# Performance work log

Measured on AMD Instinct MI355X. Metric: run time of the kernel, lower is better.

## Reference

```python
import jax, jax.numpy as jnp
import numpy as np

NUM_HEADS = 16
ROPE_BASE = 10000.0


def _rope_cos_sin(seq_len, head_dim, dtype):
    # half-split RoPE tables, shape [1, S, 1, head_dim]
    inv_freq = 1.0 / (ROPE_BASE ** (jnp.arange(0, head_dim, 2, dtype=jnp.float32) / head_dim))
    ang = jnp.arange(seq_len, dtype=jnp.float32)[:, None] * inv_freq[None, :]  # [S, hd/2]
    cos = jnp.concatenate([jnp.cos(ang), jnp.cos(ang)], axis=-1)[None, :, None, :]
    sin = jnp.concatenate([jnp.sin(ang), jnp.sin(ang)], axis=-1)[None, :, None, :]
    return cos.astype(dtype), sin.astype(dtype)


def _rotate_half(t):
    h = t.shape[-1] // 2
    return jnp.concatenate([-t[..., h:], t[..., :h]], axis=-1)


def setup_inputs() -> dict:
    key = jax.random.key(0)
    ks = jax.random.split(key, 5)
    B, S, D = 2, 2048, 1024
    std = 1.0 / np.sqrt(D)
    return {
        "x": jax.random.normal(ks[0], (B, S, D), dtype=jnp.float32),
        "Wqkv": jax.random.normal(ks[1], (D, 3 * D), dtype=jnp.float32) * std,
        "bqkv": jax.random.normal(ks[2], (3 * D,), dtype=jnp.float32) * 0.02,
        "Wproj": jax.random.normal(ks[3], (D, D), dtype=jnp.float32) * std,
        "bproj": jax.random.normal(ks[4], (D,), dtype=jnp.float32) * 0.02,
    }


def reference(x, Wqkv, bqkv, Wproj, bproj):
    B, S, D = x.shape
    H = NUM_HEADS
    hd = D // H
    scale = hd ** (-0.5)

    # fused QKV projection, then split: [B, S, 3, H, hd]
    qkv = (jnp.einsum("bsd,de->bse", x, Wqkv) + bqkv).reshape(B, S, 3, H, hd)
    q, k, v = qkv[:, :, 0], qkv[:, :, 1], qkv[:, :, 2]  # each [B, S, H, hd]

    # rotary embedding on q, k
    cos, sin = _rope_cos_sin(S, hd, x.dtype)
    q = q * cos + _rotate_half(q) * sin
    k = k * cos + _rotate_half(k) * sin

    # scaled dot-product attention (non-causal, matching flash-attn default here)
    scores = jnp.einsum("bqhd,bkhd->bhqk", q, k) * scale  # [B, H, S, S]
    probs = jax.nn.softmax(scores, axis=-1)
    o = jnp.einsum("bhqk,bkhd->bqhd", probs, v).reshape(B, S, D)

    # output projection
    return jnp.einsum("bsd,de->bse", o, Wproj) + bproj
```

## Files before the change

### kernel.cpp

```cpp
#include <hip/hip_runtime.h>

typedef unsigned short u16;
typedef unsigned int   u32;
typedef __bf16 bf16x8 __attribute__((ext_vector_type(8)));
typedef float  f32x4  __attribute__((ext_vector_type(4)));
typedef float  f32x16 __attribute__((ext_vector_type(16)));
typedef u32    u32x4  __attribute__((ext_vector_type(4)));

__device__ __forceinline__ u16 f2bf(float f) {
  u32 u = __builtin_bit_cast(u32, f);
  u += 0x7fffu + ((u >> 16) & 1u);
  return (u16)(u >> 16);
}

#define GLOAD_LDS16(gptr, lptr)                                              \
  __builtin_amdgcn_global_load_lds(                                          \
      (const __attribute__((address_space(1))) void*)(gptr),                 \
      (__attribute__((address_space(3))) void*)(lptr), 16, 0, 0)

__global__ __launch_bounds__(256) void cast_x_kernel(const float* __restrict__ x,
                                                     u16* __restrict__ xb, int n4) {
  int i = blockIdx.x * 256 + threadIdx.x;
  if (i >= n4) return;
  const float4 v = ((const float4*)x)[i];
  uint2 o;
  o.x = (u32)f2bf(v.x) | ((u32)f2bf(v.y) << 16);
  o.y = (u32)f2bf(v.z) | ((u32)f2bf(v.w) << 16);
  ((uint2*)xb)[i] = o;
}

__global__ __launch_bounds__(256) void transpose_cast_kernel(const float* __restrict__ W,
                                                             u16* __restrict__ Wt,
                                                             int K, int N) {
  __shared__ float tile[32][33];
  const int k0 = blockIdx.y * 32, n0 = blockIdx.x * 32;
  const int tx = threadIdx.x & 31, ty = threadIdx.x >> 5;
#pragma unroll
  for (int i = 0; i < 32; i += 8)
    tile[ty + i][tx] = W[(size_t)(k0 + ty + i) * N + n0 + tx];
  __syncthreads();
#pragma unroll
  for (int i = 0; i < 32; i += 8)
    Wt[(size_t)(n0 + ty + i) * K + k0 + tx] = f2bf(tile[tx][ty + i]);
}

__global__ __launch_bounds__(256) void gemm_bias_kernel(const u16* __restrict__ A,
                                                        const u16* __restrict__ Bt,
                                                        const float* __restrict__ bias,
                                                        float* __restrict__ C,
                                                        int M, int N, int K) {
  __shared__ u16 As[128][64];
  __shared__ u16 Bs[128][64];
  const int bm = blockIdx.y, bn = blockIdx.x;
  const int tid = threadIdx.x;
  const int wave = tid >> 6, lane = tid & 63;
  const int wr = wave >> 1, wc = wave & 1;
  const int l15 = lane & 15, lhi = lane >> 4;
  f32x4 acc[4][4] = {};

  const size_t arow0 = (size_t)bm * 128, brow0 = (size_t)bn * 128;
  const int srow_in = lane >> 3;
  const int sslot   = (lane & 7) ^ srow_in;

  for (int k0 = 0; k0 < K; k0 += 64) {
#pragma unroll
    for (int i = 0; i < 4; i++) {
      const int r = wave * 32 + i * 8 + srow_in;
      GLOAD_LDS16(A  + (arow0 + r) * K + k0 + sslot * 8, &As[wave * 32 + i * 8][0]);
      GLOAD_LDS16(Bt + (brow0 + r) * K + k0 + sslot * 8, &Bs[wave * 32 + i * 8][0]);
    }
    __syncthreads();

    bf16x8 af[4][2], bfr[4][2];
#pragma unroll
    for (int m = 0; m < 4; m++) {
      const int r = wr * 64 + m * 16 + l15;
#pragma unroll
      for (int kk = 0; kk < 2; kk++)
        af[m][kk] = *(const bf16x8*)(&As[0][0] + r * 64 + (((kk * 4 + lhi) ^ (r & 7)) * 8));
    }
#pragma unroll
    for (int n = 0; n < 4; n++) {
      const int r = wc * 64 + n * 16 + l15;
#pragma unroll
      for (int kk = 0; kk < 2; kk++)
        bfr[n][kk] = *(const bf16x8*)(&Bs[0][0] + r * 64 + (((kk * 4 + lhi) ^ (r & 7)) * 8));
    }
#pragma unroll
    for (int m = 0; m < 4; m++)
#pragma unroll
      for (int n = 0; n < 4; n++) {
        acc[m][n] = __builtin_amdgcn_mfma_f32_16x16x32_bf16(af[m][0], bfr[n][0], acc[m][n], 0, 0, 0);
        acc[m][n] = __builtin_amdgcn_mfma_f32_16x16x32_bf16(af[m][1], bfr[n][1], acc[m][n], 0, 0, 0);
      }
    __syncthreads();
  }
#pragma unroll
  for (int n = 0; n < 4; n++) {
    int col = bn * 128 + wc * 64 + n * 16 + l15;
    float bv = bias[col];
#pragma unroll
    for (int m = 0; m < 4; m++)
#pragma unroll
      for (int r = 0; r < 4; r++) {
        int row = bm * 128 + wr * 64 + m * 16 + lhi * 4 + r;
        C[(size_t)row * N + col] = acc[m][n][r] + bv;
      }
  }
}

#define QK_FOLD 0.18033688011112042f
__global__ __launch_bounds__(256) void rope_qk_kernel(const float* __restrict__ qkv,
                                                      u16* __restrict__ qb,
                                                      u16* __restrict__ kb) {
  const int bs = blockIdx.x;
  const int s = bs & 2047, b = bs >> 11;
  const float* base = qkv + (size_t)bs * 3072;
#pragma unroll
  for (int p = threadIdx.x; p < 512; p += 256) {
    const int h = p >> 5, i = p & 31;
    float inv = exp2f(-13.287712379549449f * (float)i * (1.0f / 32.0f));
    float ang = (float)s * inv;
    float sn, cs;
    sincosf(ang, &sn, &cs);
    float q0 = base[h * 64 + i], q1 = base[h * 64 + i + 32];
    float k0 = base[1024 + h * 64 + i], k1 = base[1024 + h * 64 + i + 32];
    size_t o = ((size_t)(b * 16 + h) * 2048 + s) * 64;
    qb[o + i]      = f2bf((q0 * cs - q1 * sn) * QK_FOLD);
    qb[o + i + 32] = f2bf((q1 * cs + q0 * sn) * QK_FOLD);
    kb[o + i]      = f2bf(k0 * cs - k1 * sn);
    kb[o + i + 32] = f2bf(k1 * cs + k0 * sn);
  }
}

__global__ __launch_bounds__(256) void v_trans_kernel(const float* __restrict__ qkv,
                                                      u16* __restrict__ vt) {
  __shared__ u16 tile[64][65];
  const int blk = blockIdx.x;
  const int st = blk & 31, h = (blk >> 5) & 15, b = blk >> 9;
  const int s0 = st * 64;
  const int t = threadIdx.x;
  const int r = t >> 2, c0 = (t & 3) * 16;
  const float* src = qkv + (size_t)(b * 2048 + s0 + r) * 3072 + 2048 + h * 64 + c0;
#pragma unroll
  for (int j = 0; j < 16; j++) tile[r][c0 + j] = f2bf(src[j]);
  __syncthreads();
  u16* dst = vt + ((size_t)(b * 16 + h) * 64 + r) * 2048 + s0 + c0;
#pragma unroll
  for (int j = 0; j < 16; j++) dst[j] = tile[c0 + j][r];
}

__global__ __launch_bounds__(256) void flash_attn_kernel(const u16* __restrict__ qg,
                                                         const u16* __restrict__ kg,
                                                         const u16* __restrict__ vg,
                                                         u16* __restrict__ og) {
  __shared__ u16 Ks[2][64][64];
  __shared__ u16 Vs[2][64][64];
  const int hw = blockIdx.x;
  const int lb = (hw & 7) * 64 + (hw >> 3);
  const int qt = lb & 15, bh = lb >> 4;
  const int b = bh >> 4, h = bh & 15;
  const int tid = threadIdx.x, wave = tid >> 6, lane = tid & 63;
  const int l5 = lane & 31, hi = lane >> 5;

  const u16* qrow = qg + ((size_t)bh * 2048 + qt * 128 + wave * 32 + l5) * 64 + hi * 8;
  bf16x8 qf[4];
#pragma unroll
  for (int kc = 0; kc < 4; kc++) qf[kc] = *(const bf16x8*)(qrow + kc * 16);

  f32x16 o[2] = {};
  float m_run = -1e30f, l_run = 0.f;

  const u16* gK = kg + (size_t)bh * 2048 * 64;
  const u16* gV = vg + (size_t)bh * 64 * 2048;
  const int srow0 = tid >> 3, sc16 = tid & 7;
  int4 kreg[2], vreg[2];

#pragma unroll
  for (int i = 0; i < 2; i++) {
    int r = srow0 + i * 32;
    kreg[i] = *(const int4*)(gK + (size_t)r * 64 + sc16 * 8);
    vreg[i] = *(const int4*)(gV + (size_t)r * 2048 + sc16 * 8);
  }
#pragma unroll
  for (int i = 0; i < 2; i++) {
    int r = srow0 + i * 32;
    int byo = r * 128 + ((sc16 * 16) ^ ((r & 7) << 4));
    *(int4*)((char*)&Ks[0][0][0] + byo) = kreg[i];
    *(int4*)((char*)&Vs[0][0][0] + byo) = vreg[i];
  }

  for (int kt = 0; kt < 32; kt++) {
    const int cur = kt & 1;
    __syncthreads();
    if (kt < 31) {
#pragma unroll
      for (int i = 0; i < 2; i++) {
        int r = srow0 + i * 32;
        kreg[i] = *(const int4*)(gK + ((size_t)(kt + 1) * 64 + r) * 64 + sc16 * 8);
        vreg[i] = *(const int4*)(gV + (size_t)r * 2048 + (kt + 1) * 64 + sc16 * 8);
      }
    }
    const char* KsB = (const char*)&Ks[cur][0][0];
    const char* VsB = (const char*)&Vs[cur][0][0];

    f32x16 sf[2];
#pragma unroll
    for (int k32 = 0; k32 < 2; k32++) {
      int r = k32 * 32 + l5;
      const char* rowp = KsB + r * 128;
      int sw = (r & 7) << 4;
      f32x16 s = {};
#pragma unroll
      for (int kc = 0; kc < 4; kc++) {
        bf16x8 kf = *(const bf16x8*)(rowp + ((kc * 32 + hi * 16) ^ sw));
        s = __builtin_amdgcn_mfma_f32_32x32x16_bf16(kf, qf[kc], s, 0, 0, 0);
      }
      sf[k32] = s;
    }

    float pmax = sf[0][0];
#pragma unroll
    for (int r = 1; r < 16; r++) pmax = fmaxf(pmax, sf[0][r]);
#pragma unroll
    for (int r = 0; r < 16; r++) pmax = fmaxf(pmax, sf[1][r]);
    pmax = fmaxf(pmax, __shfl_xor(pmax, 32));
    float mnew = fmaxf(m_run, pmax);
    float alpha = __builtin_amdgcn_exp2f(m_run - mnew);
    m_run = mnew;
    float rs = 0.f;
#pragma unroll
    for (int k32 = 0; k32 < 2; k32++)
#pragma unroll
      for (int r = 0; r < 16; r++) {
        float p = __builtin_amdgcn_exp2f(sf[k32][r] - mnew);
        sf[k32][r] = p;
        rs += p;
      }
    rs += __shfl_xor(rs, 32);
    l_run = l_run * alpha + rs;
#pragma unroll
    for (int dc = 0; dc < 2; dc++)
#pragma unroll
      for (int r = 0; r < 16; r++) o[dc][r] *= alpha;

    bf16x8 pf[4];
#pragma unroll
    for (int k32 = 0; k32 < 2; k32++) {
      u32 u[8];
#pragma unroll
      for (int m = 0; m < 8; m++) {
        u32 w;
        asm("v_cvt_pk_bf16_f32 %0, %1, %2" : "=v"(w) : "v"(sf[k32][2 * m]), "v"(sf[k32][2 * m + 1]));
        u[m] = w;
      }
      asm("v_permlane32_swap_b32 %0, %1" : "+v"(u[0]), "+v"(u[2]));
      asm("v_permlane32_swap_b32 %0, %1" : "+v"(u[1]), "+v"(u[3]));
      asm("v_permlane32_swap_b32 %0, %1" : "+v"(u[4]), "+v"(u[6]));
      asm("v_permlane32_swap_b32 %0, %1" : "+v"(u[5]), "+v"(u[7]));
      u32x4 w0 = {u[0], u[1], u[2], u[3]};
      u32x4 w1 = {u[4], u[5], u[6], u[7]};
      pf[k32 * 2]     = __builtin_bit_cast(bf16x8, w0);
      pf[k32 * 2 + 1] = __builtin_bit_cast(bf16x8, w1);
    }

#pragma unroll
    for (int dc = 0; dc < 2; dc++) {
      int r = dc * 32 + l5;
      const char* rowp = VsB + r * 128;
      int sw = (r & 7) << 4;
#pragma unroll
      for (int kc = 0; kc < 4; kc++) {
        bf16x8 vf = *(const bf16x8*)(rowp + ((kc * 32 + hi * 16) ^ sw));
        o[dc] = __builtin_amdgcn_mfma_f32_32x32x16_bf16(vf, pf[kc], o[dc], 0, 0, 0);
      }
    }

    if (kt < 31) {
#pragma unroll
      for (int i = 0; i < 2; i++) {
        int r = srow0 + i * 32;
        int byo = r * 128 + ((sc16 * 16) ^ ((r & 7) << 4));
        *(int4*)((char*)&Ks[cur ^ 1][0][0] + byo) = kreg[i];
        *(int4*)((char*)&Vs[cur ^ 1][0][0] + byo) = vreg[i];
      }
    }
  }

  float rinv = 1.0f / l_run;
  int qglob = qt * 128 + wave * 32 + l5;
  u16* orow = og + ((size_t)b * 2048 + qglob) * 1024 + h * 64;
#pragma unroll
  for (int dc = 0; dc < 2; dc++)
#pragma unroll
    for (int m = 0; m < 4; m++) {
      int d0 = dc * 32 + m * 8 + hi * 4;
      float a0 = o[dc][4 * m + 0] * rinv, a1 = o[dc][4 * m + 1] * rinv;
      float a2 = o[dc][4 * m + 2] * rinv, a3 = o[dc][4 * m + 3] * rinv;
      uint2 w;
      w.x = (u32)f2bf(a0) | ((u32)f2bf(a1) << 16);
      w.y = (u32)f2bf(a2) | ((u32)f2bf(a3) << 16);
      *(uint2*)(orow + d0) = w;
    }
}

extern "C" void kernel_launch(void* const* d_in, const int* in_sizes, int n_in,
                              void* d_out, int out_size, void* d_ws, size_t ws_size,
                              hipStream_t stream) {
  const float* x     = (const float*)d_in[0];
  const float* Wqkv  = (const float*)d_in[1];
  const float* bqkv  = (const float*)d_in[2];
  const float* Wproj = (const float*)d_in[3];
  const float* bproj = (const float*)d_in[4];
  float* out = (float*)d_out;

  char* ws = (char*)d_ws;
  u16*   xb    = (u16*)ws;
  u16*   wqkvt = xb + (size_t)4096 * 1024;
  u16*   wprot = wqkvt + (size_t)3072 * 1024;
  float* qkv   = (float*)(ws + (size_t)16 * 1024 * 1024);
  u16*   qb2   = (u16*)(ws + (size_t)64 * 1024 * 1024);
  u16*   kb2   = (u16*)(ws + (size_t)72 * 1024 * 1024);
  u16*   vtw   = (u16*)(ws + (size_t)80 * 1024 * 1024);
  u16*   obw   = (u16*)(ws + (size_t)88 * 1024 * 1024);

  cast_x_kernel<<<dim3(4096), dim3(256), 0, stream>>>(x, xb, 1048576);
  transpose_cast_kernel<<<dim3(96, 32), dim3(256), 0, stream>>>(Wqkv, wqkvt, 1024, 3072);
  transpose_cast_kernel<<<dim3(32, 32), dim3(256), 0, stream>>>(Wproj, wprot, 1024, 1024);
  gemm_bias_kernel<<<dim3(24, 32), dim3(256), 0, stream>>>(xb, wqkvt, bqkv, qkv, 4096, 3072, 1024);
  rope_qk_kernel<<<dim3(4096), dim3(256), 0, stream>>>(qkv, qb2, kb2);
  v_trans_kernel<<<dim3(1024), dim3(256), 0, stream>>>(qkv, vtw);
  flash_attn_kernel<<<dim3(512), dim3(256), 0, stream>>>(qb2, kb2, vtw, obw);
  gemm_bias_kernel<<<dim3(8, 32), dim3(256), 0, stream>>>(obw, wprot, bproj, out, 4096, 1024, 1024);
}
```

Baseline: 140.8 us.

## Fuse RoPE, bias and V transpose into QKV GEMM epilogue

The QKV GEMM epilogue now adds bias, applies RoPE with the softmax scale fold to Q/K, and writes bf16 Q, K and transposed V directly. This removes the fp32 qkv intermediate and the separate rope and V-transpose kernels. The sin/cos values come from a small precomputed table kernel instead of per-element sincos. The tradeoff is scattered 2-byte stores in the epilogue, where each lane writes separate elements.

```diff
diff --git a/kernel.cpp b/kernel.cpp
--- a/kernel.cpp
+++ b/kernel.cpp
@@ -17,6 +17,8 @@
   __builtin_amdgcn_global_load_lds(                                          \
       (const __attribute__((address_space(1))) void*)(gptr),                 \
       (__attribute__((address_space(3))) void*)(lptr), 16, 0, 0)
+
+#define QK_FOLD 0.18033688011112042f
 
 __global__ __launch_bounds__(256) void cast_x_kernel(const float* __restrict__ x,
                                                      u16* __restrict__ xb, int n4) {
@@ -42,6 +44,117 @@
 #pragma unroll
   for (int i = 0; i < 32; i += 8)
     Wt[(size_t)(n0 + ty + i) * K + k0 + tx] = f2bf(tile[tx][ty + i]);
+}
+
+__global__ __launch_bounds__(256) void rope_table_kernel(float* __restrict__ cost,
+                                                         float* __restrict__ sint) {
+  const int idx = blockIdx.x * 256 + threadIdx.x;
+  const int s = idx >> 5, i = idx & 31;
+  float inv = exp2f(-13.287712379549449f * (float)i * (1.0f / 32.0f));
+  float sn, cs;
+  sincosf((float)s * inv, &sn, &cs);
+  cost[idx] = cs;
+  sint[idx] = sn;
+}
+
+__global__ __launch_bounds__(256) void gemm_qkv_rope_kernel(const u16* __restrict__ A,
+                                                            const u16* __restrict__ Bt,
+                                                            const float* __restrict__ bias,
+                                                            const float* __restrict__ cost,
+                                                            const float* __restrict__ sint,
+                                                            u16* __restrict__ qb,
+                                                            u16* __restrict__ kb,
+                                                            u16* __restrict__ vt) {
+  __shared__ u16 As[128][64];
+  __shared__ u16 Bs[128][64];
+  const int bm = blockIdx.y, bn = blockIdx.x;
+  const int tid = threadIdx.x;
+  const int wave = tid >> 6, lane = tid & 63;
+  const int wr = wave >> 1, wc = wave & 1;
+  const int l15 = lane & 15, lhi = lane >> 4;
+  f32x4 acc[4][4] = {};
+  const int K = 1024;
+
+  const size_t arow0 = (size_t)bm * 128, brow0 = (size_t)bn * 128;
+  const int srow_in = lane >> 3;
+  const int sslot   = (lane & 7) ^ srow_in;
+
+  for (int k0 = 0; k0 < K; k0 += 64) {
+#pragma unroll
+    for (int i = 0; i < 4; i++) {
+      const int r = wave * 32 + i * 8 + srow_in;
+      GLOAD_LDS16(A  + (arow0 + r) * K + k0 + sslot * 8, &As[wave * 32 + i * 8][0]);
+      GLOAD_LDS16(Bt + (brow0 + r) * K + k0 + sslot * 8, &Bs[wave * 32 + i * 8][0]);
+    }
+    __syncthreads();
+
+    bf16x8 af[4][2], bfr[4][2];
+#pragma unroll
+    for (int m = 0; m < 4; m++) {
+      const int r = wr * 64 + m * 16 + l15;
+#pragma unroll
+      for (int kk = 0; kk < 2; kk++)
+        af[m][kk] = *(const bf16x8*)(&As[0][0] + r * 64 + (((kk * 4 + lhi) ^ (r & 7)) * 8));
+    }
+#pragma unroll
+    for (int n = 0; n < 4; n++) {
+      const int r = wc * 64 + n * 16 + l15;
+#pragma unroll
+      for (int kk = 0; kk < 2; kk++)
+        bfr[n][kk] = *(const bf16x8*)(&Bs[0][0] + r * 64 + (((kk * 4 + lhi) ^ (r & 7)) * 8));
+    }
+#pragma unroll
+    for (int m = 0; m < 4; m++)
+#pragma unroll
+      for (int n = 0; n < 4; n++) {
+        acc[m][n] = __builtin_amdgcn_mfma_f32_16x16x32_bf16(af[m][0], bfr[n][0], acc[m][n], 0, 0, 0);
+        acc[m][n] = __builtin_amdgcn_mfma_f32_16x16x32_bf16(af[m][1], bfr[n][1], acc[m][n], 0, 0, 0);
+      }
+    __syncthreads();
+  }
+
+  float bv[4];
+#pragma unroll
+  for (int n = 0; n < 4; n++) bv[n] = bias[bn * 128 + wc * 64 + n * 16 + l15];
+
+  if (bn < 16) {
+    const bool isq = bn < 8;
+    u16* dst = isq ? qb : kb;
+    const int hcol = bn * 2 + wc - (isq ? 0 : 16);
+    const float fold = isq ? QK_FOLD : 1.0f;
+#pragma unroll
+    for (int m = 0; m < 4; m++)
+#pragma unroll
+      for (int r = 0; r < 4; r++) {
+        const int row = bm * 128 + wr * 64 + m * 16 + lhi * 4 + r;
+        const int b = row >> 11, s = row & 2047;
+        const float cs0 = cost[s * 32 + l15],      sn0 = sint[s * 32 + l15];
+        const float cs1 = cost[s * 32 + 16 + l15], sn1 = sint[s * 32 + 16 + l15];
+        const float q0 = acc[m][0][r] + bv[0], q1 = acc[m][2][r] + bv[2];
+        const float q2 = acc[m][1][r] + bv[1], q3 = acc[m][3][r] + bv[3];
+        u16* orow = dst + ((size_t)(b * 16 + hcol) * 2048 + s) * 64;
+        orow[l15]      = f2bf((q0 * cs0 - q1 * sn0) * fold);
+        orow[l15 + 32] = f2bf((q1 * cs0 + q0 * sn0) * fold);
+        orow[l15 + 16] = f2bf((q2 * cs1 - q3 * sn1) * fold);
+        orow[l15 + 48] = f2bf((q3 * cs1 + q2 * sn1) * fold);
+      }
+  } else {
+    const int hcol = bn * 2 + wc - 32;
+    const int b = bm >> 4;
+#pragma unroll
+    for (int n = 0; n < 4; n++) {
+      const int d = n * 16 + l15;
+      u16* dcol = vt + ((size_t)(b * 16 + hcol) * 64 + d) * 2048;
+#pragma unroll
+      for (int m = 0; m < 4; m++) {
+        const int s = (bm * 128 + wr * 64 + m * 16 + lhi * 4) & 2047;
+        uint2 w;
+        w.x = (u32)f2bf(acc[m][n][0] + bv[n]) | ((u32)f2bf(acc[m][n][1] + bv[n]) << 16);
+        w.y = (u32)f2bf(acc[m][n][2] + bv[n]) | ((u32)f2bf(acc[m][n][3] + bv[n]) << 16);
+        *(uint2*)(dcol + s) = w;
+      }
+    }
+  }
 }
 
 __global__ __launch_bounds__(256) void gemm_bias_kernel(const u16* __restrict__ A,
@@ -98,56 +211,15 @@
 #pragma unroll
   for (int n = 0; n < 4; n++) {
     int col = bn * 128 + wc * 64 + n * 16 + l15;
-    float bv = bias[col];
+    float bvv = bias[col];
 #pragma unroll
     for (int m = 0; m < 4; m++)
 #pragma unroll
       for (int r = 0; r < 4; r++) {
         int row = bm * 128 + wr * 64 + m * 16 + lhi * 4 + r;
-        C[(size_t)row * N + col] = acc[m][n][r] + bv;
-      }
-  }
-}
-
-#define QK_FOLD 0.18033688011112042f
-__global__ __launch_bounds__(256) void rope_qk_kernel(const float* __restrict__ qkv,
-                                                      u16* __restrict__ qb,
-                                                      u16* __restrict__ kb) {
-  const int bs = blockIdx.x;
-  const int s = bs & 2047, b = bs >> 11;
-  const float* base = qkv + (size_t)bs * 3072;
-#pragma unroll
-  for (int p = threadIdx.x; p < 512; p += 256) {
-    const int h = p >> 5, i = p & 31;
-    float inv = exp2f(-13.287712379549449f * (float)i * (1.0f / 32.0f));
-    float ang = (float)s * inv;
-    float sn, cs;
-    sincosf(ang, &sn, &cs);
-    float q0 = base[h * 64 + i], q1 = base[h * 64 + i + 32];
-    float k0 = base[1024 + h * 64 + i], k1 = base[1024 + h * 64 + i + 32];
-    size_t o = ((size_t)(b * 16 + h) * 2048 + s) * 64;
-    qb[o + i]      = f2bf((q0 * cs - q1 * sn) * QK_FOLD);
-    qb[o + i + 32] = f2bf((q1 * cs + q0 * sn) * QK_FOLD);
-    kb[o + i]      = f2bf(k0 * cs - k1 * sn);
-    kb[o + i + 32] = f2bf(k1 * cs + k0 * sn);
-  }
-}
-
-__global__ __launch_bounds__(256) void v_trans_kernel(const float* __restrict__ qkv,
-                                                      u16* __restrict__ vt) {
-  __shared__ u16 tile[64][65];
-  const int blk = blockIdx.x;
-  const int st = blk & 31, h = (blk >> 5) & 15, b = blk >> 9;
-  const int s0 = st * 64;
-  const int t = threadIdx.x;
-  const int r = t >> 2, c0 = (t & 3) * 16;
-  const float* src = qkv + (size_t)(b * 2048 + s0 + r) * 3072 + 2048 + h * 64 + c0;
-#pragma unroll
-  for (int j = 0; j < 16; j++) tile[r][c0 + j] = f2bf(src[j]);
-  __syncthreads();
-  u16* dst = vt + ((size_t)(b * 16 + h) * 64 + r) * 2048 + s0 + c0;
-#pragma unroll
-  for (int j = 0; j < 16; j++) dst[j] = tile[c0 + j][r];
+        C[(size_t)row * N + col] = acc[m][n][r] + bvv;
+      }
+  }
 }
 
 __global__ __launch_bounds__(256) void flash_attn_kernel(const u16* __restrict__ qg,
@@ -318,7 +390,8 @@
   u16*   xb    = (u16*)ws;
   u16*   wqkvt = xb + (size_t)4096 * 1024;
   u16*   wprot = wqkvt + (size_t)3072 * 1024;
-  float* qkv   = (float*)(ws + (size_t)16 * 1024 * 1024);
+  float* cost  = (float*)(ws + (size_t)16 * 1024 * 1024);
+  float* sint  = cost + 2048 * 32;
   u16*   qb2   = (u16*)(ws + (size_t)64 * 1024 * 1024);
   u16*   kb2   = (u16*)(ws + (size_t)72 * 1024 * 1024);
   u16*   vtw   = (u16*)(ws + (size_t)80 * 1024 * 1024);
@@ -327,9 +400,9 @@
   cast_x_kernel<<<dim3(4096), dim3(256), 0, stream>>>(x, xb, 1048576);
   transpose_cast_kernel<<<dim3(96, 32), dim3(256), 0, stream>>>(Wqkv, wqkvt, 1024, 3072);
   transpose_cast_kernel<<<dim3(32, 32), dim3(256), 0, stream>>>(Wproj, wprot, 1024, 1024);
-  gemm_bias_kernel<<<dim3(24, 32), dim3(256), 0, stream>>>(xb, wqkvt, bqkv, qkv, 4096, 3072, 1024);
-  rope_qk_kernel<<<dim3(4096), dim3(256), 0, stream>>>(qkv, qb2, kb2);
-  v_trans_kernel<<<dim3(1024), dim3(256), 0, stream>>>(qkv, vtw);
+  rope_table_kernel<<<dim3(256), dim3(256), 0, stream>>>(cost, sint);
+  gemm_qkv_rope_kernel<<<dim3(24, 32), dim3(256), 0, stream>>>(xb, wqkvt, bqkv, cost, sint,
+                                                               qb2, kb2, vtw);
   flash_attn_kernel<<<dim3(512), dim3(256), 0, stream>>>(qb2, kb2, vtw, obw);
   gemm_bias_kernel<<<dim3(8, 32), dim3(256), 0, stream>>>(obw, wprot, bproj, out, 4096, 1024, 1024);
 }
```

Measured after the change: 140.3 us. About the same (-0.3%).
